# Optimization experiments

Measured on AMD Instinct MI355X. Metric: run time of the kernel, lower is better.

The kernel has to match this reference:

```python
import jax, jax.numpy as jnp
import numpy as np

B, N, C = 4, 1024, 512
H = 8
HD = C // H
SCALE = HD ** (-0.5)


def setup_inputs() -> dict:
    key = jax.random.key(0)
    ks = jax.random.split(key, 12)
    s = 0.02
    return {
        "x": jax.random.normal(ks[0], (B, N, C), dtype=jnp.float32),
        "y": jax.random.normal(ks[1], (B, N, C), dtype=jnp.float32),
        "Wqkv1": jax.random.normal(ks[2], (4 * C, C), dtype=jnp.float32) * s,
        "Wqkv2": jax.random.normal(ks[3], (4 * C, C), dtype=jnp.float32) * s,
        "W1": jax.random.normal(ks[4], (C, C), dtype=jnp.float32) * s,
        "b1": jnp.zeros((C,), dtype=jnp.float32),
        "W2": jax.random.normal(ks[5], (C, C), dtype=jnp.float32) * s,
        "b2": jnp.zeros((C,), dtype=jnp.float32),
        "W3": jax.random.normal(ks[6], (C, C), dtype=jnp.float32) * s,
        "b3": jnp.zeros((C,), dtype=jnp.float32),
        "W4": jax.random.normal(ks[7], (C, C), dtype=jnp.float32) * s,
        "b4": jnp.zeros((C,), dtype=jnp.float32),
    }


def _l2norm(t, eps=1e-12):
    # matches F.normalize(dim=-1)
    n = jnp.sqrt(jnp.sum(t * t, axis=-1, keepdims=True))
    return t / jnp.maximum(n, eps)


def _ortho_loss(q, qt):
    # q, qt: [B, H, N, HD]
    qn = _l2norm(q)
    qtn = _l2norm(qt)
    prod = jnp.einsum("bhnd,bhmd->bhnm", qn, qtn)  # [B,H,N,N]
    eye = jnp.eye(N, dtype=prod.dtype)
    off = prod * (1.0 - eye)
    # fro-norm squared of off-diagonal, divided by B*N*N (as in source)
    return jnp.sum(off * off) / (B * N * N)


def _qkv(inp, W):
    # inp: [B,N,C], W: [4C, C] -> [4, B, H, N, HD]
    t = (inp @ W.T).reshape(B, N, 4, H, HD)
    return jnp.transpose(t, (2, 0, 3, 1, 4))


def _attn(q, k, v):
    # q,k,v: [B,H,N,HD] -> [B,N,C]
    scores = jnp.einsum("bhnd,bhmd->bhnm", q, k) * SCALE
    a = jax.nn.softmax(scores, axis=-1)
    o = jnp.einsum("bhnm,bhmd->bhnd", a, v)
    return jnp.transpose(o, (0, 2, 1, 3)).reshape(B, N, C)


def reference(x, y, Wqkv1, Wqkv2, W1, b1, W2, b2, W3, b3, W4, b4):
    qkv1 = _qkv(x, Wqkv1)
    qkv2 = _qkv(y, Wqkv2)
    qx, kx, vx, qtx = qkv1[0], qkv1[1], qkv1[2], qkv1[3]
    qy, ky, vy, qty = qkv2[0], qkv2[1], qkv2[2], qkv2[3]

    lorthx = _ortho_loss(qx, qtx)
    lorthy = _ortho_loss(qy, qty)

    yc = _attn(qx, ky, vy)  # attncy @ vy
    xc = _attn(qy, kx, vx)  # attncx @ vx
    xt = _attn(qtx, kx, vx)
    yt = _attn(qty, ky, vy)

    xc = xc @ W1.T + b1
    yc = yc @ W2.T + b2
    xt = xt @ W3.T + b3
    yt = yt @ W4.T + b4

    # pairwise cosine distance between normalized xc, yc
    xcn = _l2norm(xc)
    ycn = _l2norm(yc)
    cos = jnp.sum(xcn * ycn, axis=-1)
    lc = jnp.mean(1.0 - cos)

    return (xc, yc, xt, yt, lorthx, lorthy, lc)
```

## Files before the change

### kernel.cpp

```cpp
#include <hip/hip_runtime.h>

typedef unsigned short u16;
typedef __attribute__((ext_vector_type(4))) unsigned short u16x4;
typedef __attribute__((ext_vector_type(8))) unsigned short u16x8;
typedef __attribute__((ext_vector_type(4))) float          f32x4;
typedef __attribute__((ext_vector_type(8))) __bf16         bf16x8;

#define MFMA16(a,b,c) __builtin_amdgcn_mfma_f32_16x16x32_bf16((a),(b),(c),0,0,0)
#define SCALE 0.125f

__device__ __forceinline__ u16 f2b(float f){
  unsigned u = __builtin_bit_cast(unsigned, f);
  u = (u + 0x7fffu + ((u >> 16) & 1u)) >> 16;
  return (u16)u;
}
__device__ __forceinline__ u16 f2b_trunc(float f){
  return (u16)(__builtin_bit_cast(unsigned, f) >> 16);
}
__device__ __forceinline__ float b2f(u16 v){
  unsigned u = ((unsigned)v) << 16;
  return __builtin_bit_cast(float, u);
}
__device__ __forceinline__ void async16(const u16* g, u16* l){
  __builtin_amdgcn_global_load_lds(
      (const __attribute__((address_space(1))) unsigned*)g,
      (__attribute__((address_space(3))) unsigned*)l, 16, 0, 0);
}
__device__ __forceinline__ int swz(int row, int chunk, int off){
  return row*64 + (((chunk ^ row ^ (row >> 3)) & 7) << 3) + off;
}

__global__ void cast_all_k(const float* __restrict__ x, const float* __restrict__ y,
                           const float* __restrict__ wq1, const float* __restrict__ wq2,
                           const float* __restrict__ w1, const float* __restrict__ w2,
                           const float* __restrict__ w3, const float* __restrict__ w4,
                           u16* __restrict__ dst){
  int i = blockIdx.x * 256 + threadIdx.x;
  const float* s; int base;
  if      (i < 524288)  { s = x;   base = 0;       }
  else if (i < 1048576) { s = y;   base = 524288;  }
  else if (i < 1310720) { s = wq1; base = 1048576; }
  else if (i < 1572864) { s = wq2; base = 1310720; }
  else if (i < 1638400) { s = w1;  base = 1572864; }
  else if (i < 1703936) { s = w2;  base = 1638400; }
  else if (i < 1769472) { s = w3;  base = 1703936; }
  else                  { s = w4;  base = 1769472; }
  float4 v = ((const float4*)s)[i - base];
  u16x4 o; o[0]=f2b(v.x); o[1]=f2b(v.y); o[2]=f2b(v.z); o[3]=f2b(v.w);
  ((u16x4*)dst)[i] = o;
}

__global__ __launch_bounds__(256, 2) void qkv_mega_k(
    const u16* __restrict__ xb, const u16* __restrict__ Wq,
    u16* __restrict__ qkv, u16* __restrict__ vT)
{
  const int i = blockIdx.x;
  const u16 *A, *B; u16* C; int ldc, m0, n0;
  if (i < 512) {
    int z = i >> 8, t = i & 255;
    m0 = (t & 31)*128; n0 = (t >> 5)*128;
    A = xb + (size_t)z*2097152; B = Wq + (size_t)z*1048576;
    C = qkv + (size_t)z*8388608; ldc = 2048;
  } else if (i < 768) {
    int z = (i-512) >> 7, t = (i-512) & 127;
    m0 = (t & 31)*128; n0 = (t >> 5)*128;
    A = xb + (size_t)z*2097152; B = Wq + (size_t)z*1048576 + (size_t)1536*512;
    C = qkv + (size_t)z*8388608 + 1536; ldc = 2048;
  } else {
    int z = (i-768) >> 7, t = (i-768) & 127;
    m0 = (t & 3)*128; n0 = (t >> 2)*128;
    A = Wq + (size_t)z*1048576 + (size_t)1024*512; B = xb + (size_t)z*2097152;
    C = vT + (size_t)z*2097152; ldc = 4096;
  }

  __shared__ u16 As[128*32];
  __shared__ u16 Bs[128*32];
  const int tid  = threadIdx.x;
  const int w    = tid >> 6, lane = tid & 63;
  const int quad = lane >> 4, l16 = lane & 15;
  const int wr   = w >> 1, wc = w & 1;

  f32x4 acc[4][4] = {};
  const int rowa = lane >> 2;
  const int ko   = (lane & 3) * 8;

  for (int k0 = 0; k0 < 512; k0 += 32) {
    __syncthreads();
#pragma unroll
    for (int r = 0; r < 2; ++r) {
      int rb = (r*4 + w) * 16;
      async16(A + (size_t)(m0 + rb + rowa)*512 + k0 + ko, As + (r*4 + w)*512);
      async16(B + (size_t)(n0 + rb + rowa)*512 + k0 + ko, Bs + (r*4 + w)*512);
    }
    __syncthreads();
    bf16x8 af[4], bfr[4];
#pragma unroll
    for (int ii = 0; ii < 4; ++ii)
      af[ii] = *(const bf16x8*)&As[(wr*64 + ii*16 + l16)*32 + quad*8];
#pragma unroll
    for (int j = 0; j < 4; ++j)
      bfr[j] = *(const bf16x8*)&Bs[(wc*64 + j*16 + l16)*32 + quad*8];
#pragma unroll
    for (int ii = 0; ii < 4; ++ii)
#pragma unroll
      for (int j = 0; j < 4; ++j)
        acc[ii][j] = MFMA16(af[ii], bfr[j], acc[ii][j]);
  }
#pragma unroll
  for (int j = 0; j < 4; ++j) {
    int col = n0 + wc*64 + j*16 + l16;
#pragma unroll
    for (int ii = 0; ii < 4; ++ii)
#pragma unroll
      for (int reg = 0; reg < 4; ++reg) {
        int row = m0 + wr*64 + ii*16 + quad*4 + reg;
        C[(size_t)row*ldc + col] = f2b(acc[ii][j][reg]);
      }
  }
}

__global__ __launch_bounds__(256, 2) void gemm_fin_k(
    const u16* __restrict__ A0, size_t aStr, const u16* __restrict__ B0, size_t bStr,
    const float* __restrict__ bias0, const float* __restrict__ bias1,
    const float* __restrict__ bias2, const float* __restrict__ bias3,
    float* __restrict__ C0, size_t cStr)
{
  const int z = blockIdx.z;
  const u16* A = A0 + (size_t)z * aStr;
  const u16* Bm = B0 + (size_t)z * bStr;
  float* Cb = C0 + (size_t)z * cStr;
  const float* bias = (z==0) ? bias0 : (z==1) ? bias1 : (z==2) ? bias2 : bias3;

  __shared__ u16 As[128*32];
  __shared__ u16 Bs[128*32];
  const int tid  = threadIdx.x;
  const int w    = tid >> 6, lane = tid & 63;
  const int quad = lane >> 4, l16 = lane & 15;
  const int wr   = w >> 1, wc = w & 1;
  const int m0 = blockIdx.x * 128, n0 = blockIdx.y * 128;

  f32x4 acc[4][4] = {};
  const int rowa = lane >> 2;
  const int ko   = (lane & 3) * 8;

  for (int k0 = 0; k0 < 512; k0 += 32) {
    __syncthreads();
#pragma unroll
    for (int r = 0; r < 2; ++r) {
      int rb = (r*4 + w) * 16;
      async16(A  + (size_t)(m0 + rb + rowa)*512 + k0 + ko, As + (r*4 + w)*512);
      async16(Bm + (size_t)(n0 + rb + rowa)*512 + k0 + ko, Bs + (r*4 + w)*512);
    }
    __syncthreads();
    bf16x8 af[4], bfr[4];
#pragma unroll
    for (int ii = 0; ii < 4; ++ii)
      af[ii] = *(const bf16x8*)&As[(wr*64 + ii*16 + l16)*32 + quad*8];
#pragma unroll
    for (int j = 0; j < 4; ++j)
      bfr[j] = *(const bf16x8*)&Bs[(wc*64 + j*16 + l16)*32 + quad*8];
#pragma unroll
    for (int ii = 0; ii < 4; ++ii)
#pragma unroll
      for (int j = 0; j < 4; ++j)
        acc[ii][j] = MFMA16(af[ii], bfr[j], acc[ii][j]);
  }
#pragma unroll
  for (int j = 0; j < 4; ++j) {
    int col = n0 + wc*64 + j*16 + l16;
    float bv = bias[col];
#pragma unroll
    for (int ii = 0; ii < 4; ++ii)
#pragma unroll
      for (int reg = 0; reg < 4; ++reg) {
        int row = m0 + wr*64 + ii*16 + quad*4 + reg;
        Cb[(size_t)row*512 + col] = acc[ii][j][reg] + bv;
      }
  }
}

__global__ __launch_bounds__(256, 2) void attn_k(
    const u16* __restrict__ qkv1, const u16* __restrict__ qkv2,
    const u16* __restrict__ vT1, const u16* __restrict__ vT2,
    u16* __restrict__ ao)
{
  const int qt = blockIdx.x, bh = blockIdx.y, p = blockIdx.z;
  const int b = bh >> 3, h = bh & 7;
  const u16* kvsrc = p ? qkv2 : qkv1;
  const u16* vsrc  = p ? vT2 : vT1;
  const u16* qsrcA = p ? qkv1 : qkv2;  const int qoffA = h*64;
  const u16* qsrcB = p ? qkv2 : qkv1;  const int qoffB = 1536 + h*64;
  const int koff = 512 + h*64;
  const size_t tb = (size_t)b * 1024;

  __shared__ u16 Ks[2][4096];
  __shared__ u16 Vt[2][4096];
  __shared__ u16 Ps[4][1024];

  const int tid = threadIdx.x, w = tid >> 6, lane = tid & 63;
  const int quad = lane >> 4, l16 = lane & 15;
  const int srow = tid >> 3, sch = tid & 7;

  bf16x8 qb[2][2][2];
#pragma unroll
  for (int s2 = 0; s2 < 2; ++s2) {
    size_t row = tb + qt*128 + w*32 + s2*16 + l16;
    const u16* qrA = qsrcA + row*2048 + qoffA;
    const u16* qrB = qsrcB + row*2048 + qoffB;
    qb[0][s2][0] = *(const bf16x8*)(qrA + quad*8);
    qb[0][s2][1] = *(const bf16x8*)(qrA + 32 + quad*8);
    qb[1][s2][0] = *(const bf16x8*)(qrB + quad*8);
    qb[1][s2][1] = *(const bf16x8*)(qrB + 32 + quad*8);
  }

  f32x4 oacc[2][2][4] = {};
  float lp[2][2] = {};
  u16* myP = Ps[w];

  u16x8 kreg[2], vreg[2];
  auto loadTile = [&](int t){
#pragma unroll
    for (int r = 0; r < 2; ++r) {
      kreg[r] = *(const u16x8*)(kvsrc + (tb + t*64 + r*32 + srow)*2048 + koff + sch*8);
      vreg[r] = *(const u16x8*)(vsrc + (size_t)(h*64 + r*32 + srow)*4096 + tb + t*64 + sch*8);
    }
  };
  auto storeTile = [&](int buf){
#pragma unroll
    for (int r = 0; r < 2; ++r) {
      *(u16x8*)&Ks[buf][swz(r*32 + srow, sch, 0)] = kreg[r];
      *(u16x8*)&Vt[buf][swz(r*32 + srow, sch, 0)] = vreg[r];
    }
  };

  loadTile(0);
  storeTile(0);
  loadTile(1);

  for (int kt = 0; kt < 16; ++kt) {
    const int cur = kt & 1;
    __syncthreads();
    if (kt < 15) storeTile(cur ^ 1);
    if (kt < 14) loadTile(kt + 2);

    bf16x8 ka[4][2], vb[4][2];
#pragma unroll
    for (int j = 0; j < 4; ++j) {
      ka[j][0] = *(const bf16x8*)&Ks[cur][swz(j*16 + l16, quad, 0)];
      ka[j][1] = *(const bf16x8*)&Ks[cur][swz(j*16 + l16, quad + 4, 0)];
      vb[j][0] = *(const bf16x8*)&Vt[cur][swz(j*16 + l16, quad, 0)];
      vb[j][1] = *(const bf16x8*)&Vt[cur][swz(j*16 + l16, quad + 4, 0)];
    }

#pragma unroll
    for (int o = 0; o < 2; ++o)
#pragma unroll
      for (int s2 = 0; s2 < 2; ++s2) {
#pragma unroll
        for (int j = 0; j < 4; ++j) {
          f32x4 t = {};
          t = MFMA16(ka[j][0], qb[o][s2][0], t);
          t = MFMA16(ka[j][1], qb[o][s2][1], t);
          u16x4 pk;
#pragma unroll
          for (int reg = 0; reg < 4; ++reg) {
            float pv = __expf(t[reg] * SCALE);
            lp[o][s2] += pv;
            pk[reg] = f2b_trunc(pv);
          }
          *(u16x4*)&myP[swz(l16, j*2 + (quad >> 1), (quad & 1)*4)] = pk;
        }
        bf16x8 pa0 = *(const bf16x8*)&myP[swz(l16, quad, 0)];
        bf16x8 pa1 = *(const bf16x8*)&myP[swz(l16, quad + 4, 0)];
#pragma unroll
        for (int j = 0; j < 4; ++j) {
          oacc[o][s2][j] = MFMA16(pa0, vb[j][0], oacc[o][s2][j]);
          oacc[o][s2][j] = MFMA16(pa1, vb[j][1], oacc[o][s2][j]);
        }
      }
  }

#pragma unroll
  for (int o = 0; o < 2; ++o) {
    int a = p + o*2;
    u16* aop = ao + (size_t)a*(4096*512) + (tb + qt*128)*512 + h*64;
#pragma unroll
    for (int s2 = 0; s2 < 2; ++s2) {
      float lt = lp[o][s2];
      lt += __shfl_xor(lt, 16);
      lt += __shfl_xor(lt, 32);
#pragma unroll
      for (int reg = 0; reg < 4; ++reg) {
        float lrow = __shfl(lt, quad*4 + reg);
        float linv = 1.f / lrow;
        int row = w*32 + s2*16 + quad*4 + reg;
#pragma unroll
        for (int j = 0; j < 4; ++j)
          aop[(size_t)row*512 + j*16 + l16] = f2b(oacc[o][s2][j][reg] * linv);
      }
    }
  }
}

__global__ __launch_bounds__(256, 2) void orthoA_k(
    const u16* __restrict__ qkv1, const u16* __restrict__ qkv2,
    float* __restrict__ Gbuf, float* __restrict__ accum)
{
  const int bh = blockIdx.x, which = blockIdx.y, tg = blockIdx.z;
  const u16* src = which ? qkv2 : qkv1;
  const int b = bh >> 3, h = bh & 7;
  const size_t tb = (size_t)b * 1024;

  __shared__ u16 QnT[4096], QtnT[4096];
  const int tid = threadIdx.x, w = tid >> 6, lane = tid & 63;
  const int quad = lane >> 4, l16 = lane & 15;

  f32x4 gq[4] = {}, gqt[4] = {};
  float diag = 0.f;

  for (int tt = 0; tt < 2; ++tt) {
    int t = tg*2 + tt;
    __syncthreads();
    if (tid < 128) {
      int tok = tid & 63, mat = tid >> 6;
      const u16* pp = src + (tb + t*64 + tok)*2048 + (mat ? 1536 : 0) + h*64;
      u16x8 rowv[8];
#pragma unroll
      for (int i = 0; i < 8; ++i) rowv[i] = *(const u16x8*)(pp + i*8);
      float ss = 0.f;
#pragma unroll
      for (int i = 0; i < 8; ++i)
#pragma unroll
        for (int jj = 0; jj < 8; ++jj) { float f = b2f(rowv[i][jj]); ss += f*f; }
      float inv = 1.f / fmaxf(sqrtf(ss), 1e-12f);
      u16* dst = mat ? QtnT : QnT;
#pragma unroll
      for (int i = 0; i < 8; ++i)
#pragma unroll
        for (int jj = 0; jj < 8; ++jj)
          dst[swz(i*8 + jj, tok >> 3, tok & 7)] = f2b(b2f(rowv[i][jj]) * inv);
      if (mat == 0) {
        const u16* p2 = src + (tb + t*64 + tok)*2048 + 1536 + h*64;
        float ss2 = 0.f, dot = 0.f;
#pragma unroll
        for (int i = 0; i < 8; ++i) {
          u16x8 r2 = *(const u16x8*)(p2 + i*8);
#pragma unroll
          for (int jj = 0; jj < 8; ++jj) {
            float fq = b2f(rowv[i][jj]), ft = b2f(r2[jj]);
            ss2 += ft*ft; dot += fq*ft;
          }
        }
        float inv2 = 1.f / fmaxf(sqrtf(ss2), 1e-12f);
        float dn = dot * inv * inv2;
        diag += dn * dn;
      }
    }
    __syncthreads();
    bf16x8 a0 = *(const bf16x8*)&QnT [swz(w*16 + l16, quad, 0)];
    bf16x8 a1 = *(const bf16x8*)&QnT [swz(w*16 + l16, quad + 4, 0)];
    bf16x8 t0 = *(const bf16x8*)&QtnT[swz(w*16 + l16, quad, 0)];
    bf16x8 t1 = *(const bf16x8*)&QtnT[swz(w*16 + l16, quad + 4, 0)];
#pragma unroll
    for (int j = 0; j < 4; ++j) {
      bf16x8 b0 = *(const bf16x8*)&QnT [swz(j*16 + l16, quad, 0)];
      bf16x8 b1 = *(const bf16x8*)&QnT [swz(j*16 + l16, quad + 4, 0)];
      gq[j]  = MFMA16(a0, b0, gq[j]);
      gq[j]  = MFMA16(a1, b1, gq[j]);
      bf16x8 c0 = *(const bf16x8*)&QtnT[swz(j*16 + l16, quad, 0)];
      bf16x8 c1 = *(const bf16x8*)&QtnT[swz(j*16 + l16, quad + 4, 0)];
      gqt[j] = MFMA16(t0, c0, gqt[j]);
      gqt[j] = MFMA16(t1, c1, gqt[j]);
    }
  }
  float* Gq = Gbuf + (size_t)((which*32 + bh)*2) * 4096;
  float* Gt = Gq + 4096;
#pragma unroll
  for (int j = 0; j < 4; ++j)
#pragma unroll
    for (int reg = 0; reg < 4; ++reg) {
      int row = w*16 + quad*4 + reg, col = j*16 + l16;
      atomicAdd(&Gq[row*64 + col], gq[j][reg]);
      atomicAdd(&Gt[row*64 + col], gqt[j][reg]);
    }
  if (tid < 64) atomicAdd(&accum[which], -diag);
}

__global__ __launch_bounds__(256, 2) void red_k(
    const float* __restrict__ Gbuf, const float* __restrict__ dout,
    float* __restrict__ accum)
{
  const int tid = threadIdx.x;
  if (blockIdx.x < 64) {
    const int w = tid >> 6, lane = tid & 63;
    const int wid = blockIdx.x * 4 + w;
    float acc = 0.f;
    for (int rr = 0; rr < 16; ++rr) {
      int row = wid*16 + rr;
      const float4* xr = (const float4*)(dout + (size_t)row*512 + lane*8);
      const float4* yr = (const float4*)(dout + 2097152 + (size_t)row*512 + lane*8);
      float4 x0 = xr[0], x1 = xr[1], y0 = yr[0], y1 = yr[1];
      float dxy = x0.x*y0.x + x0.y*y0.y + x0.z*y0.z + x0.w*y0.w
                + x1.x*y1.x + x1.y*y1.y + x1.z*y1.z + x1.w*y1.w;
      float sx  = x0.x*x0.x + x0.y*x0.y + x0.z*x0.z + x0.w*x0.w
                + x1.x*x1.x + x1.y*x1.y + x1.z*x1.z + x1.w*x1.w;
      float sy  = y0.x*y0.x + y0.y*y0.y + y0.z*y0.z + y0.w*y0.w
                + y1.x*y1.x + y1.y*y1.y + y1.z*y1.z + y1.w*y1.w;
#pragma unroll
      for (int off = 32; off > 0; off >>= 1) {
        dxy += __shfl_xor(dxy, off);
        sx  += __shfl_xor(sx,  off);
        sy  += __shfl_xor(sy,  off);
      }
      if (lane == 0) {
        float cosv = dxy / (fmaxf(sqrtf(sx), 1e-12f) * fmaxf(sqrtf(sy), 1e-12f));
        acc += 1.f - cosv;
      }
    }
    if (lane == 0) atomicAdd(&accum[2], acc);
  } else {
    const int i = blockIdx.x - 64;
    const int bh = i & 31, which = i >> 5;
    const float* Gq = Gbuf + (size_t)((which*32 + bh)*2) * 4096;
    const float* Gt = Gq + 4096;
    float acc = 0.f;
    for (int idx = tid*4; idx < 4096; idx += 1024) {
      float4 g  = *(const float4*)(Gq + idx);
      float4 gt = *(const float4*)(Gt + idx);
      acc += g.x*gt.x + g.y*gt.y + g.z*gt.z + g.w*gt.w;
    }
    __shared__ float red[256];
    red[tid] = acc; __syncthreads();
    for (int s2 = 128; s2 > 0; s2 >>= 1) {
      if (tid < s2) red[tid] += red[tid + s2];
      __syncthreads();
    }
    if (tid == 0) atomicAdd(&accum[which], red[0]);
  }
}

__global__ void fin_k(const float* __restrict__ accum, float* __restrict__ outs){
  if (threadIdx.x == 0) {
    outs[0] = accum[0] * (1.f/4194304.f);
    outs[1] = accum[1] * (1.f/4194304.f);
    outs[2] = accum[2] * (1.f/4096.f);
  }
}

extern "C" void kernel_launch(void* const* d_in, const int* in_sizes, int n_in,
                              void* d_out, int out_size, void* d_ws, size_t ws_size,
                              hipStream_t stream)
{
  (void)in_sizes; (void)n_in; (void)out_size; (void)ws_size;
  const float* x     = (const float*)d_in[0];
  const float* y     = (const float*)d_in[1];
  const float* Wqkv1 = (const float*)d_in[2];
  const float* Wqkv2 = (const float*)d_in[3];
  const float* W1 = (const float*)d_in[4];
  const float* b1 = (const float*)d_in[5];
  const float* W2 = (const float*)d_in[6];
  const float* b2 = (const float*)d_in[7];
  const float* W3 = (const float*)d_in[8];
  const float* b3 = (const float*)d_in[9];
  const float* W4 = (const float*)d_in[10];
  const float* b4 = (const float*)d_in[11];

  u16* ws   = (u16*)d_ws;
  u16* xb   = ws;
  u16* Wq1b = ws + (size_t)4194304;
  u16* W1b  = ws + (size_t)6291456;
  u16* qkv1 = ws + (size_t)7340032;
  u16* qkv2 = qkv1 + (size_t)8388608;
  u16* aob  = qkv2 + (size_t)8388608;
  float* accum = (float*)(aob + (size_t)8388608);
  float* Gbuf  = accum + 16;
  u16* vT1 = (u16*)d_out;
  u16* vT2 = vT1 + (size_t)2097152;

  hipMemsetAsync(accum, 0, 16, stream);
  hipMemsetAsync(Gbuf, 0, 2097152, stream);

  cast_all_k<<<dim3(7168), dim3(256), 0, stream>>>(x, y, Wqkv1, Wqkv2, W1, W2, W3, W4, xb);

  qkv_mega_k<<<dim3(1024), dim3(256), 0, stream>>>(xb, Wq1b, qkv1, vT1);

  attn_k<<<dim3(8,32,2), 256, 0, stream>>>(qkv1, qkv2, vT1, vT2, aob);

  orthoA_k<<<dim3(32,2,8), 256, 0, stream>>>(qkv1, qkv2, Gbuf, accum);

  float* outb = (float*)d_out;
  gemm_fin_k<<<dim3(32,4,4), 256, 0, stream>>>(
      aob, 2097152, W1b, 262144, b1, b2, b3, b4, outb, 2097152);

  red_k<<<dim3(128), 256, 0, stream>>>(Gbuf, outb, accum);
  fin_k<<<dim3(1), dim3(64), 0, stream>>>(accum, outb + 8388608);
}
```

Baseline: 236.7 us.

## Fold softmax scale into Q weights, use exp2, and compute row sums via MFMA

```diff
diff --git a/kernel.cpp b/kernel.cpp
--- a/kernel.cpp
+++ b/kernel.cpp
@@ -8,6 +8,7 @@
 
 #define MFMA16(a,b,c) __builtin_amdgcn_mfma_f32_16x16x32_bf16((a),(b),(c),0,0,0)
 #define SCALE 0.125f
+#define SCALE_LOG2E 0.18033688011112042f
 
 __device__ __forceinline__ u16 f2b(float f){
   unsigned u = __builtin_bit_cast(unsigned, f);
@@ -36,17 +37,19 @@
                            const float* __restrict__ w3, const float* __restrict__ w4,
                            u16* __restrict__ dst){
   int i = blockIdx.x * 256 + threadIdx.x;
-  const float* s; int base;
+  const float* s; int base; float sc = 1.f;
   if      (i < 524288)  { s = x;   base = 0;       }
   else if (i < 1048576) { s = y;   base = 524288;  }
-  else if (i < 1310720) { s = wq1; base = 1048576; }
-  else if (i < 1572864) { s = wq2; base = 1310720; }
+  else if (i < 1310720) { s = wq1; base = 1048576;
+    int iw = i - base; if (iw < 65536 || iw >= 196608) sc = SCALE_LOG2E; }
+  else if (i < 1572864) { s = wq2; base = 1310720;
+    int iw = i - base; if (iw < 65536 || iw >= 196608) sc = SCALE_LOG2E; }
   else if (i < 1638400) { s = w1;  base = 1572864; }
   else if (i < 1703936) { s = w2;  base = 1638400; }
   else if (i < 1769472) { s = w3;  base = 1703936; }
   else                  { s = w4;  base = 1769472; }
   float4 v = ((const float4*)s)[i - base];
-  u16x4 o; o[0]=f2b(v.x); o[1]=f2b(v.y); o[2]=f2b(v.z); o[3]=f2b(v.w);
+  u16x4 o; o[0]=f2b(v.x*sc); o[1]=f2b(v.y*sc); o[2]=f2b(v.z*sc); o[3]=f2b(v.w*sc);
   ((u16x4*)dst)[i] = o;
 }
 
@@ -201,6 +204,11 @@
   const int quad = lane >> 4, l16 = lane & 15;
   const int srow = tid >> 3, sch = tid & 7;
 
+  u16x8 onesu;
+#pragma unroll
+  for (int ii = 0; ii < 8; ++ii) onesu[ii] = 0x3f80;
+  const bf16x8 ONES = __builtin_bit_cast(bf16x8, onesu);
+
   bf16x8 qb[2][2][2];
 #pragma unroll
   for (int s2 = 0; s2 < 2; ++s2) {
@@ -214,7 +222,7 @@
   }
 
   f32x4 oacc[2][2][4] = {};
-  float lp[2][2] = {};
+  f32x4 lacc[2][2] = {};
   u16* myP = Ps[w];
 
   u16x8 kreg[2], vreg[2];
@@ -259,24 +267,27 @@
 #pragma unroll
         for (int j = 0; j < 4; ++j) {
           f32x4 t = {};
+          __builtin_amdgcn_s_setprio(1);
           t = MFMA16(ka[j][0], qb[o][s2][0], t);
           t = MFMA16(ka[j][1], qb[o][s2][1], t);
+          __builtin_amdgcn_s_setprio(0);
           u16x4 pk;
 #pragma unroll
-          for (int reg = 0; reg < 4; ++reg) {
-            float pv = __expf(t[reg] * SCALE);
-            lp[o][s2] += pv;
-            pk[reg] = f2b_trunc(pv);
-          }
+          for (int reg = 0; reg < 4; ++reg)
+            pk[reg] = f2b_trunc(__builtin_amdgcn_exp2f(t[reg]));
           *(u16x4*)&myP[swz(l16, j*2 + (quad >> 1), (quad & 1)*4)] = pk;
         }
         bf16x8 pa0 = *(const bf16x8*)&myP[swz(l16, quad, 0)];
         bf16x8 pa1 = *(const bf16x8*)&myP[swz(l16, quad + 4, 0)];
+        __builtin_amdgcn_s_setprio(1);
 #pragma unroll
         for (int j = 0; j < 4; ++j) {
           oacc[o][s2][j] = MFMA16(pa0, vb[j][0], oacc[o][s2][j]);
           oacc[o][s2][j] = MFMA16(pa1, vb[j][1], oacc[o][s2][j]);
         }
+        lacc[o][s2] = MFMA16(pa0, ONES, lacc[o][s2]);
+        lacc[o][s2] = MFMA16(pa1, ONES, lacc[o][s2]);
+        __builtin_amdgcn_s_setprio(0);
       }
   }
 
@@ -286,13 +297,9 @@
     u16* aop = ao + (size_t)a*(4096*512) + (tb + qt*128)*512 + h*64;
 #pragma unroll
     for (int s2 = 0; s2 < 2; ++s2) {
-      float lt = lp[o][s2];
-      lt += __shfl_xor(lt, 16);
-      lt += __shfl_xor(lt, 32);
 #pragma unroll
       for (int reg = 0; reg < 4; ++reg) {
-        float lrow = __shfl(lt, quad*4 + reg);
-        float linv = 1.f / lrow;
+        float linv = 1.f / lacc[o][s2][reg];
         int row = w*32 + s2*16 + quad*4 + reg;
 #pragma unroll
         for (int j = 0; j < 4; ++j)
```

Result: faster. 231.3 us (-2.3%).
